# Kernel tuning notes

Hardware: AMD Instinct MI355X
Metric: run time of the kernel (lower is better)

The kernel has to match this reference:

```python
import jax, jax.numpy as jnp
import numpy as np

BATCH, IN_DIM, H, W = 16, 32, 128, 128
BASE_OUT = 32


def setup_inputs() -> dict:
    key = jax.random.key(0)
    k_x, k_w2, k_b2, k_w1, k_b1 = jax.random.split(key, 5)
    x = jax.random.normal(k_x, (BATCH, IN_DIM, H, W), dtype=jnp.float32)
    # Conv2d(input_dim, 4*base_out, 1): weight (4bo, in_dim) after squeezing 1x1 kernel
    s2 = 1.0 / np.sqrt(IN_DIM)
    W2 = jax.random.uniform(k_w2, (4 * BASE_OUT, IN_DIM), jnp.float32, -s2, s2)
    b2 = jax.random.uniform(k_b2, (4 * BASE_OUT,), jnp.float32, -s2, s2)
    # Conv1d(base_out, 4*base_out, 2): weight (4bo, bo, 2)
    s1 = 1.0 / np.sqrt(BASE_OUT * 2)
    W1 = jax.random.uniform(k_w1, (4 * BASE_OUT, BASE_OUT, 2), jnp.float32, -s1, s1)
    b1 = jax.random.uniform(k_b1, (4 * BASE_OUT,), jnp.float32, -s1, s1)
    return {"x": x, "W2": W2, "b2": b2, "W1": W1, "b1": b1}


def reference(x, W2, b2, W1, b1):
    b, c, h, w = x.shape
    bo = W1.shape[1]  # base_out
    # skew: row i of x is placed at columns [i, i+w) of a (h, 2w-1) canvas
    rows = jnp.arange(h)
    cols = rows[:, None] + jnp.arange(w)[None, :]  # (h, w)
    skewed = jnp.zeros((b, c, h, 2 * w - 1), x.dtype).at[:, :, rows[:, None], cols].set(x)
    # 1x1 conv over channels: input-to-state pre-activations
    i2s = jnp.einsum('oc,bchy->bohy', W2, skewed) + b2[None, :, None, None]
    # original loops only over the first w skewed columns
    xs = jnp.moveaxis(i2s[:, :, :, :w], 3, 0)  # (w, b, 4bo, h)
    W1_prev, W1_cur = W1[:, :, 0], W1[:, :, 1]

    def step(carry, xt):
        pc, ph = carry  # (b, bo, h) each
        # Conv1d(kernel=2) on [0, prev_h]: tap 0 sees ph shifted right by one
        ph_shift = jnp.pad(ph, ((0, 0), (0, 0), (1, 0)))[:, :, :-1]
        s2s = (jnp.einsum('oc,bch->boh', W1_prev, ph_shift)
               + jnp.einsum('oc,bch->boh', W1_cur, ph)
               + b1[None, :, None])
        g = xt + s2s
        o = jax.nn.sigmoid(g[:, 0 * bo:1 * bo])
        f = jax.nn.sigmoid(g[:, 1 * bo:2 * bo])
        i = jax.nn.sigmoid(g[:, 2 * bo:3 * bo])
        gg = jnp.tanh(g[:, 3 * bo:4 * bo])
        nc = f * pc + i * gg
        nh = o * jnp.tanh(nc)
        return (nc, nh), nh

    c0 = jnp.zeros((b, bo, h), x.dtype)
    _, hs = jax.lax.scan(step, (c0, c0), xs)  # hs: (w, b, bo, h)
    return jnp.moveaxis(hs, 0, -1)  # (b, bo, h, w)
```

## Files before the change

### kernel.cpp

```cpp
#include <hip/hip_runtime.h>
#include <stdint.h>

#define BATCH 16
#define CIN   32
#define HH    128
#define WW    128
#define BO    32
#define OCH   128
#define NCH   4
#define RPC   32
#define DEPTH 64

#define RINGMAX ((size_t)BATCH * 16 * DEPTH * BO * 8)
#define I2SHSZ  ((size_t)BATCH * WW * HH * OCH * 2)

typedef _Float16 f16x4v __attribute__((ext_vector_type(4)));
typedef _Float16 f16x8v __attribute__((ext_vector_type(8)));
typedef float    f32x4v __attribute__((ext_vector_type(4)));

__global__ __launch_bounds__(256, 4) void i2s_gemm_h(
    const float* __restrict__ x, const float* __restrict__ W2g,
    const float* __restrict__ b2, const float* __restrict__ b1,
    _Float16* __restrict__ i2sh)
{
    const int tid = threadIdx.x;
    const int bx  = blockIdx.x;
    const int b   = bx >> 7;
    const int row = bx & 127;

    __shared__ __attribute__((aligned(16))) float xs[CIN][WW];
    __shared__ __attribute__((aligned(16))) float w2s[CIN][OCH];
    __shared__ float bs[OCH];

    for (int i = tid; i < CIN * OCH; i += 256) {
        const int c = i >> 7, o = i & 127;
        w2s[c][o] = W2g[o * CIN + c];
    }
    if (tid < OCH) bs[tid] = b2[tid] + b1[tid];
    for (int i = tid; i < CIN * WW; i += 256) {
        const int c = i >> 7, t = i & 127;
        xs[c][t] = (t >= row)
            ? x[((size_t)(b * CIN + c) * HH + row) * WW + (t - row)] : 0.f;
    }
    __syncthreads();

    const int tm = tid >> 4;
    const int tn = tid & 15;
    const int t0 = tm * 8, o0 = tn * 8;

    float bv[8];
    *(float4*)&bv[0] = *(const float4*)&bs[o0];
    *(float4*)&bv[4] = *(const float4*)&bs[o0 + 4];
    float acc[8][8];
#pragma unroll
    for (int i = 0; i < 8; ++i)
#pragma unroll
        for (int jj = 0; jj < 8; ++jj) acc[i][jj] = bv[jj];

    for (int c = 0; c < CIN; ++c) {
        float a[8], wv[8];
        *(float4*)&a[0]  = *(const float4*)&xs[c][t0];
        *(float4*)&a[4]  = *(const float4*)&xs[c][t0 + 4];
        *(float4*)&wv[0] = *(const float4*)&w2s[c][o0];
        *(float4*)&wv[4] = *(const float4*)&w2s[c][o0 + 4];
#pragma unroll
        for (int i = 0; i < 8; ++i)
#pragma unroll
            for (int jj = 0; jj < 8; ++jj)
                acc[i][jj] = fmaf(a[i], wv[jj], acc[i][jj]);
    }

#pragma unroll
    for (int i = 0; i < 8; ++i) {
        f16x8v hv;
#pragma unroll
        for (int jj = 0; jj < 8; ++jj) hv[jj] = (_Float16)acc[i][jj];
        *(f16x8v*)&i2sh[((size_t)(b * WW + (t0 + i)) * HH + row) * OCH + o0] = hv;
    }
}

__global__ __launch_bounds__(256) void diag_lstm_scan_v12(
    const float* __restrict__ W1g, float* __restrict__ out,
    int* __restrict__ progress, unsigned long long* __restrict__ hand,
    const _Float16* __restrict__ i2sh)
{
    const int tid = threadIdx.x;
    const int l   = tid & 63;
    const int w   = tid >> 6;
    const int m   = w >> 1;
    const int p   = w & 1;
    const int q   = l >> 4;
    const int col = l & 15;
    const int blk = blockIdx.x;
    const int b   = blk & 15;
    const int k   = blk >> 4;

    __shared__ _Float16 phs[2][33][40];
    for (int i = tid; i < 2 * 33 * 40; i += 256) (&phs[0][0][0])[i] = (_Float16)0.f;

    f16x8v bw[4][2];
#pragma unroll
    for (int s = 0; s < 4; ++s) {
        const int o = (p + 2 * s) * 16 + col;
#pragma unroll
        for (int h = 0; h < 2; ++h) {
            const float4 w0 = *(const float4*)&W1g[(size_t)o * 64 + 32 * h + 8 * q];
            const float4 w1 = *(const float4*)&W1g[(size_t)o * 64 + 32 * h + 8 * q + 4];
            f16x8v v;
            v[0] = (_Float16)w0.x; v[1] = (_Float16)w0.y;
            v[2] = (_Float16)w0.z; v[3] = (_Float16)w0.w;
            v[4] = (_Float16)w1.x; v[5] = (_Float16)w1.y;
            v[6] = (_Float16)w1.z; v[7] = (_Float16)w1.w;
            bw[s][h] = v;
        }
    }

    const ushort* i2su = (const ushort*)i2sh;
    const int j = 16 * p + col;
    const int grow0 = k * RPC + 16 * m + 4 * q;
    ushort u[4][4];
    {
        const size_t base = ((size_t)(b * WW + 0) * HH + grow0) * OCH + j;
#pragma unroll
        for (int s = 0; s < 4; ++s)
#pragma unroll
            for (int e = 0; e < 4; ++e)
                u[s][e] = i2su[base + (size_t)e * OCH + 32 * s];
    }

    float pc[4] = {0.f, 0.f, 0.f, 0.f};

    const int kprev = (k > 0) ? k - 1 : 0;
    const unsigned long long* srcring =
        hand + ((size_t)(b * NCH + kprev) * DEPTH) * BO + l;
    unsigned long long* dstring =
        hand + ((size_t)(b * NCH + k) * DEPTH) * BO + j;
    int* myprog   = progress + (b * NCH + k);
    int* consprog = myprog + 1;
    unsigned long long pre = 0ull;

    __syncthreads();

    for (int t = 0; t < WW; ++t) {
        _Float16 (*PS)[40] = phs[t & 1];
        _Float16 (*PD)[40] = phs[(t & 1) ^ 1];

        if (m == 0 && k > 0 && t > 0) {
            unsigned long long qv = pre;
            while (__any(l < 32 && (unsigned)(qv >> 32) != (unsigned)t)) {
                if (l < 32)
                    qv = __hip_atomic_load(&srcring[(size_t)((t - 1) & 63) * BO],
                                           __ATOMIC_RELAXED, __HIP_MEMORY_SCOPE_AGENT);
            }
            if (l < 32) {
                PS[0][l] = (_Float16)__uint_as_float((unsigned)qv);
                pre = __hip_atomic_load(&srcring[(size_t)(t & 63) * BO],
                                        __ATOMIC_RELAXED, __HIP_MEMORY_SCOPE_AGENT);
            }
        }

        const f16x4v r0 = *(const f16x4v*)&PS[16 * m + col][4 * q];
        const f16x4v r1 = *(const f16x4v*)&PS[16 * m + col + 1][4 * q];
        const f16x4v r2 = *(const f16x4v*)&PS[16 * m + col][16 + 4 * q];
        const f16x4v r3 = *(const f16x4v*)&PS[16 * m + col + 1][16 + 4 * q];
        f16x8v af0, af1;
        af0[0] = r0[0]; af0[1] = r1[0]; af0[2] = r0[1]; af0[3] = r1[1];
        af0[4] = r0[2]; af0[5] = r1[2]; af0[6] = r0[3]; af0[7] = r1[3];
        af1[0] = r2[0]; af1[1] = r3[0]; af1[2] = r2[1]; af1[3] = r3[1];
        af1[4] = r2[2]; af1[5] = r3[2]; af1[6] = r2[3]; af1[7] = r3[3];

        f32x4v acc[4];
#pragma unroll
        for (int s = 0; s < 4; ++s)
#pragma unroll
            for (int e = 0; e < 4; ++e) {
                ushort uv = u[s][e];
                acc[s][e] = (float)(*reinterpret_cast<const _Float16*>(&uv));
            }
        {
            const int tn = (t + 1 < WW) ? t + 1 : WW - 1;
            const size_t base = ((size_t)(b * WW + tn) * HH + grow0) * OCH + j;
#pragma unroll
            for (int s = 0; s < 4; ++s)
#pragma unroll
                for (int e = 0; e < 4; ++e)
                    u[s][e] = i2su[base + (size_t)e * OCH + 32 * s];
        }

#pragma unroll
        for (int s = 0; s < 4; ++s) {
            acc[s] = __builtin_amdgcn_mfma_f32_16x16x32_f16(af0, bw[s][0], acc[s], 0, 0, 0);
            acc[s] = __builtin_amdgcn_mfma_f32_16x16x32_f16(af1, bw[s][1], acc[s], 0, 0, 0);
        }

        if (m == 1 && k < NCH - 1 && l == 0 && (t & 15) == 0 && t >= 48) {
            while (__hip_atomic_load(consprog, __ATOMIC_RELAXED,
                                     __HIP_MEMORY_SCOPE_AGENT) < t - 39) { }
        }

#pragma unroll
        for (int e = 0; e < 4; ++e) {
            const float go = acc[0][e];
            const float gf = acc[1][e];
            const float gi = acc[2][e];
            const float gg = acc[3][e];
            const float so = 1.f / (1.f + __expf(-go));
            const float sf = 1.f / (1.f + __expf(-gf));
            const float si = 1.f / (1.f + __expf(-gi));
            const float tg = 2.f / (1.f + __expf(-2.f * gg)) - 1.f;
            const float nc = sf * pc[e] + si * tg;
            const float th = 2.f / (1.f + __expf(-2.f * nc)) - 1.f;
            const float nh = so * th;
            pc[e] = nc;
            PD[16 * m + 4 * q + e + 1][j] = (_Float16)nh;

            out[((size_t)(b * BO + j) * HH + (grow0 + e)) * WW + t] = nh;

            if (m == 1 && q == 3 && e == 3 && k < NCH - 1) {
                unsigned long long qq =
                    ((unsigned long long)(unsigned)(t + 1) << 32)
                  | (unsigned long long)__float_as_uint(nh);
                __hip_atomic_store(&dstring[(size_t)(t & 63) * BO], qq,
                                   __ATOMIC_RELAXED, __HIP_MEMORY_SCOPE_AGENT);
            }
        }
        if (tid == 0) {
            __hip_atomic_store(myprog, t + 1, __ATOMIC_RELAXED,
                               __HIP_MEMORY_SCOPE_AGENT);
        }
        __syncthreads();
    }
}

__global__ __launch_bounds__(512, 2) void diag_lstm_scan_v4(
    const float* __restrict__ x, const float* __restrict__ W2g,
    const float* __restrict__ b2, const float* __restrict__ W1g,
    const float* __restrict__ b1, float* __restrict__ out,
    int* __restrict__ progress, unsigned long long* __restrict__ hand)
{
    const int tid = threadIdx.x;
    const int l   = tid & 63;
    const int w   = tid >> 6;
    const int blk = blockIdx.x;
    const int b = (blk & 7) + ((blk >> 7) << 3);
    const int k = (blk >> 3) & 15;
    const int row = k * 8 + w;

    __shared__ __attribute__((aligned(16))) float phs[2][9][BO];
    __shared__ __attribute__((aligned(16))) float xbuf[8][CIN];
    __shared__ __attribute__((aligned(16))) float gbuf2[8][OCH];

    for (int i = tid; i < 2 * 9 * BO; i += 512) ((float*)phs)[i] = 0.f;

    const int o0 = 2 * l, o1 = 2 * l + 1;
    float w2a[CIN], w2b[CIN], w1pa[CIN], w1ca[CIN], w1pb[CIN], w1cb[CIN];
#pragma unroll
    for (int c = 0; c < CIN; ++c) {
        w2a[c]  = W2g[o0 * CIN + c];
        w2b[c]  = W2g[o1 * CIN + c];
        w1pa[c] = W1g[(o0 * CIN + c) * 2 + 0];
        w1ca[c] = W1g[(o0 * CIN + c) * 2 + 1];
        w1pb[c] = W1g[(o1 * CIN + c) * 2 + 0];
        w1cb[c] = W1g[(o1 * CIN + c) * 2 + 1];
    }
    const float biasA = b2[o0] + b1[o0];
    const float biasB = b2[o1] + b1[o1];

    const int j = l & 31;
    float pc = 0.f, ob0 = 0.f, ob1 = 0.f, ob2 = 0.f;
    float* outrow = out + ((size_t)(b * BO + j) * HH + row) * WW;

    const int kprev = (k > 0) ? k - 1 : 0;
    const unsigned long long* srcbase =
        hand + (size_t)((b * 16 + kprev) * DEPTH) * BO + j;
    unsigned long long* dstbase =
        hand + (size_t)((b * 16 + k) * DEPTH) * BO + j;
    int* myprog   = progress + (b * 16 + k);
    int* consprog = myprog + 1;

    unsigned long long pre = 0ull;
    __syncthreads();

    for (int t = 0; t < WW; ++t) {
        const int par = t & 1;
        if (l < 32) {
            const int wp = t - row;
            xbuf[w][l] = (wp >= 0)
                ? x[((size_t)(b * CIN + l) * HH + row) * WW + wp] : 0.f;
        }
        if (w == 0 && k > 0) {
            if (t > 0) {
                unsigned long long q = pre;
                while (__any((unsigned)(q >> 32) != (unsigned)t)) {
                    q = __hip_atomic_load(&srcbase[(size_t)((t - 1) & (DEPTH - 1)) * BO],
                                          __ATOMIC_RELAXED, __HIP_MEMORY_SCOPE_AGENT);
                }
                if (l < 32) phs[par][0][l] = __uint_as_float((unsigned)q);
            }
            pre = __hip_atomic_load(&srcbase[(size_t)(t & (DEPTH - 1)) * BO],
                                    __ATOMIC_RELAXED, __HIP_MEMORY_SCOPE_AGENT);
        }
        asm volatile("s_waitcnt lgkmcnt(0)" ::: "memory");

        float ga = biasA, gb = biasB;
        {
            const float4* xb4 = (const float4*)(&xbuf[w][0]);
            const float4* pv4 = (const float4*)(&phs[par][w][0]);
            const float4* qv4 = (const float4*)(&phs[par][w + 1][0]);
#pragma unroll
            for (int cc = 0; cc < CIN / 4; ++cc) {
                const float4 xv = xb4[cc];
                const float4 pv = pv4[cc];
                const float4 qv = qv4[cc];
                const float* xs = (const float*)&xv;
                const float* ps = (const float*)&pv;
                const float* qs = (const float*)&qv;
#pragma unroll
                for (int ci = 0; ci < 4; ++ci) {
                    const int c = 4 * cc + ci;
                    ga = fmaf(w2a[c],  xs[ci], ga);
                    gb = fmaf(w2b[c],  xs[ci], gb);
                    ga = fmaf(w1pa[c], ps[ci], ga);
                    gb = fmaf(w1pb[c], ps[ci], gb);
                    ga = fmaf(w1ca[c], qs[ci], ga);
                    gb = fmaf(w1cb[c], qs[ci], gb);
                }
            }
        }
        *(float2*)&gbuf2[w][o0] = make_float2(ga, gb);
        asm volatile("s_waitcnt lgkmcnt(0)" ::: "memory");

        if (l < 32) {
            if (w == 7 && k < 15 && (t & 15) == 0 && t >= 48) {
                while (__hip_atomic_load(consprog, __ATOMIC_RELAXED,
                                         __HIP_MEMORY_SCOPE_AGENT) < t - 47) { }
            }
            const float go = gbuf2[w][l];
            const float gf = gbuf2[w][32 + l];
            const float gi = gbuf2[w][64 + l];
            const float gg = gbuf2[w][96 + l];
            const float so = 1.f / (1.f + __expf(-go));
            const float sf = 1.f / (1.f + __expf(-gf));
            const float si = 1.f / (1.f + __expf(-gi));
            const float tg = 2.f / (1.f + __expf(-2.f * gg)) - 1.f;
            const float nc = sf * pc + si * tg;
            const float th = 2.f / (1.f + __expf(-2.f * nc)) - 1.f;
            const float nh = so * th;
            pc = nc;
            phs[par ^ 1][w + 1][l] = nh;

            const int ph4 = t & 3;
            if (ph4 == 0) ob0 = nh;
            else if (ph4 == 1) ob1 = nh;
            else if (ph4 == 2) ob2 = nh;
            else *(float4*)(outrow + (t - 3)) = make_float4(ob0, ob1, ob2, nh);

            if (w == 7 && k < 15) {
                unsigned long long q = ((unsigned long long)(unsigned)(t + 1) << 32)
                                     | (unsigned long long)__float_as_uint(nh);
                __hip_atomic_store(&dstbase[(size_t)(t & (DEPTH - 1)) * BO], q,
                                   __ATOMIC_RELAXED, __HIP_MEMORY_SCOPE_AGENT);
            }
            if (w == 0 && l == 0) {
                __hip_atomic_store(myprog, t + 1, __ATOMIC_RELAXED,
                                   __HIP_MEMORY_SCOPE_AGENT);
            }
        }
        __syncthreads();
    }
}

extern "C" void kernel_launch(void* const* d_in, const int* in_sizes, int n_in,
                              void* d_out, int out_size, void* d_ws, size_t ws_size,
                              hipStream_t stream) {
    const float* x  = (const float*)d_in[0];
    const float* W2 = (const float*)d_in[1];
    const float* b2 = (const float*)d_in[2];
    const float* W1 = (const float*)d_in[3];
    const float* b1 = (const float*)d_in[4];
    float* out = (float*)d_out;

    int* progress = (int*)d_ws;
    unsigned long long* hand = (unsigned long long*)((char*)d_ws + 4096);
    _Float16* i2sh = (_Float16*)((char*)d_ws + 4096 + RINGMAX);

    const size_t need = 4096 + RINGMAX + I2SHSZ;

    hipMemsetAsync(d_ws, 0, 4096 + RINGMAX, stream);

    if (ws_size >= need) {
        hipLaunchKernelGGL(i2s_gemm_h, dim3(BATCH * HH), dim3(256), 0, stream,
                           x, W2, b2, b1, i2sh);
        hipLaunchKernelGGL(diag_lstm_scan_v12, dim3(BATCH * NCH), dim3(256), 0, stream,
                           W1, out, progress, hand, i2sh);
    } else {
        hipLaunchKernelGGL(diag_lstm_scan_v4, dim3(BATCH * 16), dim3(512), 0, stream,
                           x, W2, b2, W1, b1, out, progress, hand);
    }
}
```

Before: 251.1 us.

## Run each batch's full diagonal LSTM scan in one 1024-thread block

The scan kernel no longer splits each batch's 128 rows across four cooperating blocks. Those blocks passed boundary hidden states through a global ring buffer with spin-waiting and progress counters. Now one 1024-thread block per batch handles all rows, and a larger shared-memory tile holds the whole column, so only __syncthreads is needed per time step. The workspace memset moves to the fallback path only. This removes cross-block handoff latency and the memset, but uses only 16 blocks and puts four times the MFMA and transcendental work on each CU per step.

New measurement: 500.6 us. +99.4%, slower.

```diff
diff --git a/kernel.cpp b/kernel.cpp
--- a/kernel.cpp
+++ b/kernel.cpp
@@ -7,8 +7,6 @@
 #define WW    128
 #define BO    32
 #define OCH   128
-#define NCH   4
-#define RPC   32
 #define DEPTH 64
 
 #define RINGMAX ((size_t)BATCH * 16 * DEPTH * BO * 8)
@@ -79,9 +77,8 @@
     }
 }
 
-__global__ __launch_bounds__(256) void diag_lstm_scan_v12(
+__global__ __launch_bounds__(1024, 4) void diag_lstm_scan_v13(
     const float* __restrict__ W1g, float* __restrict__ out,
-    int* __restrict__ progress, unsigned long long* __restrict__ hand,
     const _Float16* __restrict__ i2sh)
 {
     const int tid = threadIdx.x;
@@ -91,12 +88,11 @@
     const int p   = w & 1;
     const int q   = l >> 4;
     const int col = l & 15;
-    const int blk = blockIdx.x;
-    const int b   = blk & 15;
-    const int k   = blk >> 4;
-
-    __shared__ _Float16 phs[2][33][40];
-    for (int i = tid; i < 2 * 33 * 40; i += 256) (&phs[0][0][0])[i] = (_Float16)0.f;
+    const int b   = blockIdx.x;
+
+    __shared__ _Float16 phs[2][HH + 1][44];
+    for (int i = tid; i < 2 * (HH + 1) * 44; i += 1024)
+        (&phs[0][0][0])[i] = (_Float16)0.f;
 
     f16x8v bw[4][2];
 #pragma unroll
@@ -117,7 +113,7 @@
 
     const ushort* i2su = (const ushort*)i2sh;
     const int j = 16 * p + col;
-    const int grow0 = k * RPC + 16 * m + 4 * q;
+    const int grow0 = 16 * m + 4 * q;
     ushort u[4][4];
     {
         const size_t base = ((size_t)(b * WW + 0) * HH + grow0) * OCH + j;
@@ -130,34 +126,11 @@
 
     float pc[4] = {0.f, 0.f, 0.f, 0.f};
 
-    const int kprev = (k > 0) ? k - 1 : 0;
-    const unsigned long long* srcring =
-        hand + ((size_t)(b * NCH + kprev) * DEPTH) * BO + l;
-    unsigned long long* dstring =
-        hand + ((size_t)(b * NCH + k) * DEPTH) * BO + j;
-    int* myprog   = progress + (b * NCH + k);
-    int* consprog = myprog + 1;
-    unsigned long long pre = 0ull;
-
     __syncthreads();
 
     for (int t = 0; t < WW; ++t) {
-        _Float16 (*PS)[40] = phs[t & 1];
-        _Float16 (*PD)[40] = phs[(t & 1) ^ 1];
-
-        if (m == 0 && k > 0 && t > 0) {
-            unsigned long long qv = pre;
-            while (__any(l < 32 && (unsigned)(qv >> 32) != (unsigned)t)) {
-                if (l < 32)
-                    qv = __hip_atomic_load(&srcring[(size_t)((t - 1) & 63) * BO],
-                                           __ATOMIC_RELAXED, __HIP_MEMORY_SCOPE_AGENT);
-            }
-            if (l < 32) {
-                PS[0][l] = (_Float16)__uint_as_float((unsigned)qv);
-                pre = __hip_atomic_load(&srcring[(size_t)(t & 63) * BO],
-                                        __ATOMIC_RELAXED, __HIP_MEMORY_SCOPE_AGENT);
-            }
-        }
+        _Float16 (*PS)[44] = phs[t & 1];
+        _Float16 (*PD)[44] = phs[(t & 1) ^ 1];
 
         const f16x4v r0 = *(const f16x4v*)&PS[16 * m + col][4 * q];
         const f16x4v r1 = *(const f16x4v*)&PS[16 * m + col + 1][4 * q];
@@ -191,11 +164,6 @@
         for (int s = 0; s < 4; ++s) {
             acc[s] = __builtin_amdgcn_mfma_f32_16x16x32_f16(af0, bw[s][0], acc[s], 0, 0, 0);
             acc[s] = __builtin_amdgcn_mfma_f32_16x16x32_f16(af1, bw[s][1], acc[s], 0, 0, 0);
-        }
-
-        if (m == 1 && k < NCH - 1 && l == 0 && (t & 15) == 0 && t >= 48) {
-            while (__hip_atomic_load(consprog, __ATOMIC_RELAXED,
-                                     __HIP_MEMORY_SCOPE_AGENT) < t - 39) { }
         }
 
 #pragma unroll
@@ -212,22 +180,10 @@
             const float th = 2.f / (1.f + __expf(-2.f * nc)) - 1.f;
             const float nh = so * th;
             pc[e] = nc;
-            PD[16 * m + 4 * q + e + 1][j] = (_Float16)nh;
-
+            PD[grow0 + e + 1][j] = (_Float16)nh;
             out[((size_t)(b * BO + j) * HH + (grow0 + e)) * WW + t] = nh;
-
-            if (m == 1 && q == 3 && e == 3 && k < NCH - 1) {
-                unsigned long long qq =
-                    ((unsigned long long)(unsigned)(t + 1) << 32)
-                  | (unsigned long long)__float_as_uint(nh);
-                __hip_atomic_store(&dstring[(size_t)(t & 63) * BO], qq,
-                                   __ATOMIC_RELAXED, __HIP_MEMORY_SCOPE_AGENT);
-            }
-        }
-        if (tid == 0) {
-            __hip_atomic_store(myprog, t + 1, __ATOMIC_RELAXED,
-                               __HIP_MEMORY_SCOPE_AGENT);
-        }
+        }
+
         __syncthreads();
     }
 }
@@ -386,14 +342,13 @@
 
     const size_t need = 4096 + RINGMAX + I2SHSZ;
 
-    hipMemsetAsync(d_ws, 0, 4096 + RINGMAX, stream);
-
     if (ws_size >= need) {
         hipLaunchKernelGGL(i2s_gemm_h, dim3(BATCH * HH), dim3(256), 0, stream,
                            x, W2, b2, b1, i2sh);
-        hipLaunchKernelGGL(diag_lstm_scan_v12, dim3(BATCH * NCH), dim3(256), 0, stream,
-                           W1, out, progress, hand, i2sh);
+        hipLaunchKernelGGL(diag_lstm_scan_v13, dim3(BATCH), dim3(1024), 0, stream,
+                           W1, out, i2sh);
     } else {
+        hipMemsetAsync(d_ws, 0, 4096 + RINGMAX, stream);
         hipLaunchKernelGGL(diag_lstm_scan_v4, dim3(BATCH * 16), dim3(512), 0, stream,
                            x, W2, b2, W1, b1, out, progress, hand);
     }
```
